# Performance work log

Measured on AMD Instinct MI355X. Metric: run time of the kernel, lower is better.

The kernel has to match this reference:

```python
import jax, jax.numpy as jnp
import numpy as np

B, D, H = 32768, 256, 256
LEAKY = 0.2  # tf.nn.leaky_relu default alpha


def setup_inputs() -> dict:
    key = jax.random.key(0)
    ks = jax.random.split(key, 12)
    s = 0.05  # weight scale (original inits comm net to zeros; random keeps grads nonzero)
    return {
        "x": jax.random.normal(ks[0], (B, D), jnp.float32),
        "visible_states_indices": jax.random.randint(ks[1], (B, 1), 0, B, jnp.int32),
        "real_step": jnp.ones((1,), jnp.bool_),
        "h": jax.random.normal(ks[2], (B, H), jnp.float32),
        "c": jax.random.normal(ks[3], (B, H), jnp.float32),
        "W1": s * jax.random.normal(ks[4], (2 * H, 512), jnp.float32),
        "b1": jnp.zeros((512,), jnp.float32),
        "W2": s * jax.random.normal(ks[5], (512, 512), jnp.float32),
        "b2": jnp.zeros((512,), jnp.float32),
        "W3": s * jax.random.normal(ks[6], (512, H), jnp.float32),
        "b3": jnp.zeros((H,), jnp.float32),
        "Wk": s * jax.random.normal(ks[7], (D, 4 * H), jnp.float32),
        "Wr": s * jax.random.normal(ks[8], (H, 4 * H), jnp.float32),
        "bl": jnp.zeros((4 * H,), jnp.float32),
    }


def reference(x, visible_states_indices, real_step, h, c,
              W1, b1, W2, b2, W3, b3, Wk, Wr, bl):
    vid = jnp.squeeze(visible_states_indices, axis=1)          # [B]
    rs = jnp.reshape(real_step, ())                            # scalar bool

    # gather neighbor comm states with a pad row for idx == -1
    padded = jnp.pad(h, ((1, 0), (0, 0)))                      # [B+1, H]
    gathered = jnp.take(padded, vid + 1, axis=0)               # [B, H]

    cs = jnp.concatenate([h, gathered], axis=-1)               # [B, 2H]
    for W, b in ((W1, b1), (W2, b2), (W3, b3)):
        cs = jax.nn.leaky_relu(cs @ W + b, negative_slope=LEAKY)

    # conditional scatter-combine back into the h state
    final_h = jnp.where((vid >= 0)[:, None], h + cs, h)        # [B, H]

    # wrapped LSTM cell (keras LSTMCell gate ordering i, f, g, o)
    z = x @ Wk + final_h @ Wr + bl                             # [B, 4H]
    i, f, g, o = jnp.split(z, 4, axis=-1)
    c_new = jax.nn.sigmoid(f) * c + jax.nn.sigmoid(i) * jnp.tanh(g)
    h_new = jax.nn.sigmoid(o) * jnp.tanh(c_new)
    outputs = h_new

    # only commit new states on real steps
    h_out = jnp.where(rs, h_new, final_h)
    c_out = jnp.where(rs, c_new, c)
    return outputs, h_out, c_out
```

## Files before the change

### kernel.cpp

```cpp
#include <hip/hip_runtime.h>
#include <stdint.h>

#define LEAKY 0.2f
#define NB 32768
#define HD 256

typedef __attribute__((ext_vector_type(8))) short short8;
typedef __attribute__((ext_vector_type(8))) unsigned short ushort8;
typedef __attribute__((ext_vector_type(4))) float f4;

static __device__ __forceinline__ float bf2f(unsigned short u) {
  union { unsigned int i; float f; } v; v.i = ((unsigned int)u) << 16; return v.f;
}
static __device__ __forceinline__ unsigned short f2bf(float f) {
  union { float f; unsigned int i; } v; v.f = f;
  return (unsigned short)((v.i + 0x7fffu + ((v.i >> 16) & 1u)) >> 16);
}
static __device__ __forceinline__ ushort8 pack8(f4 a, f4 b) {
  ushort8 o;
  o[0] = f2bf(a[0]); o[1] = f2bf(a[1]); o[2] = f2bf(a[2]); o[3] = f2bf(a[3]);
  o[4] = f2bf(b[0]); o[5] = f2bf(b[1]); o[6] = f2bf(b[2]); o[7] = f2bf(b[3]);
  return o;
}
static __device__ __forceinline__ float sigm(float x) { return 1.f / (1.f + __expf(-x)); }
static __device__ __forceinline__ float tanha(float x) {
  float e = __expf(2.f * x);
  return 1.f - 2.f / (e + 1.f);
}

__device__ __forceinline__ void gload16(const void* g, void* s) {
  __builtin_amdgcn_global_load_lds(
      (const __attribute__((address_space(1))) unsigned int*)g,
      (__attribute__((address_space(3))) unsigned int*)s, 16, 0, 0);
}

__global__ void wprep(const float* __restrict__ W1, const float* __restrict__ W2,
                      const float* __restrict__ W3, const float* __restrict__ Wk,
                      const float* __restrict__ Wr,
                      unsigned short* __restrict__ W1t, unsigned short* __restrict__ W2t,
                      unsigned short* __restrict__ W3t, unsigned short* __restrict__ Wkrt) {
  __shared__ float tile[64][65];
  const int id = blockIdx.x, t = threadIdx.x;
  const int tr = t >> 6, tc = t & 63;

  const float* src;
  unsigned short* dst;
  int kbase, nbase, srcld, perm = 0;
  if (id < 64) {
    src = W1; dst = W1t; srcld = 512;
    kbase = (id >> 3) * 64; nbase = (id & 7) * 64;
  } else if (id < 128) {
    src = W2; dst = W2t; srcld = 512;
    kbase = ((id - 64) >> 3) * 64; nbase = ((id - 64) & 7) * 64;
  } else if (id < 160) {
    src = W3; dst = W3t; srcld = 256;
    kbase = ((id - 128) >> 2) * 64; nbase = ((id - 128) & 3) * 64;
  } else {
    src = nullptr; dst = Wkrt; srcld = 1024; perm = 1;
    kbase = ((id - 160) >> 4) * 64; nbase = ((id - 160) & 15) * 64;
  }

#pragma unroll
  for (int p = 0; p < 16; ++p) {
    int r = p * 4 + tr;
    int k = kbase + r, n = nbase + tc;
    float v;
    if (perm) {
      v = (k < 256) ? Wk[k * 1024 + n] : Wr[(k - 256) * 1024 + n];
    } else {
      v = src[k * srcld + n];
    }
    tile[r][tc] = v;
  }
  __syncthreads();
#pragma unroll
  for (int p = 0; p < 16; ++p) {
    int c = p * 4 + tr;
    int n = nbase + c;
    int orow;
    if (perm) {
      int gate = n >> 8, hcol = n & 255;
      orow = (hcol >> 5) * 128 + ((hcol >> 4) & 1) * 64 + gate * 16 + (hcol & 15);
    } else {
      orow = n;
    }
    dst[orow * 512 + kbase + tc] = f2bf(tile[tc][c]);
  }
}

__global__ void build_rows(const float* __restrict__ x, const float* __restrict__ h,
                           const int* __restrict__ vid,
                           unsigned short* __restrict__ catb,
                           unsigned short* __restrict__ csb) {
  int idx = blockIdx.x * 256 + threadIdx.x;
  int m = idx >> 5;
  int j = (idx & 31) << 3;
  f4 a0 = *(const f4*)(x + (size_t)m * 256 + j);
  f4 a1 = *(const f4*)(x + (size_t)m * 256 + j + 4);
  *(ushort8*)(catb + (size_t)m * 512 + j) = pack8(a0, a1);
  f4 h0 = *(const f4*)(h + (size_t)m * 256 + j);
  f4 h1 = *(const f4*)(h + (size_t)m * 256 + j + 4);
  *(ushort8*)(csb + (size_t)m * 512 + j) = pack8(h0, h1);
  int id = vid[m];
  f4 g0 = {0.f, 0.f, 0.f, 0.f}, g1 = {0.f, 0.f, 0.f, 0.f};
  if (id >= 0) {
    g0 = *(const f4*)(h + (size_t)id * 256 + j);
    g1 = *(const f4*)(h + (size_t)id * 256 + j + 4);
  }
  *(ushort8*)(csb + (size_t)m * 512 + 256 + j) = pack8(g0, g1);
}

template <int MODE, int NTN>
__global__ __launch_bounds__(256, 4) void gemm_bf16(
    const unsigned short* __restrict__ A,
    const unsigned short* __restrict__ Bt,
    const float* __restrict__ bias,
    int K,
    unsigned short* __restrict__ outb, int ldo, int col_off,
    float* __restrict__ outf,
    const float* __restrict__ hst,
    const int* __restrict__ vid,
    const float* __restrict__ cin,
    const unsigned char* __restrict__ rsp) {
  __shared__ unsigned short sA[128 * 64];
  __shared__ unsigned short sB[128 * 64];

  const int t = threadIdx.x;
  const int p = blockIdx.x;
  const int xcd = p & 7, local = p >> 3;
  const int tm = xcd + ((local / NTN) << 3);
  const int tn = local % NTN;
  const int wid = t >> 6, lane = t & 63;
  const int wr = wid >> 1, wc = wid & 1;
  const int lrow = lane & 15, lkhi = lane >> 4;

  const unsigned short* Asrc = A + (size_t)tm * 128 * K;
  const unsigned short* Bsrc = Bt + (size_t)tn * 128 * K;
  const int rsub = t >> 3, slot = t & 7;

  f4 acc[4][4];
#pragma unroll
  for (int i = 0; i < 4; ++i)
#pragma unroll
    for (int j = 0; j < 4; ++j) acc[i][j] = {0.f, 0.f, 0.f, 0.f};

  for (int k0 = 0; k0 < K; k0 += 64) {
#pragma unroll
    for (int iss = 0; iss < 4; ++iss) {
      int r = iss * 32 + rsub;
      int gs = slot ^ (r & 7);
      gload16(Asrc + (size_t)r * K + k0 + gs * 8, (char*)sA + r * 128 + slot * 16);
      gload16(Bsrc + (size_t)r * K + k0 + gs * 8, (char*)sB + r * 128 + slot * 16);
    }
    __syncthreads();
#pragma unroll
    for (int kk = 0; kk < 2; ++kk) {
      short8 af[4], bfr[4];
#pragma unroll
      for (int mi = 0; mi < 4; ++mi) {
        int row = wr * 64 + mi * 16 + lrow;
        int s = (kk * 4 + lkhi) ^ (row & 7);
        af[mi] = *(const short8*)&sA[row * 64 + s * 8];
      }
#pragma unroll
      for (int ni = 0; ni < 4; ++ni) {
        int rn = wc * 64 + ni * 16 + lrow;
        int s = (kk * 4 + lkhi) ^ (rn & 7);
        bfr[ni] = *(const short8*)&sB[rn * 64 + s * 8];
      }
#pragma unroll
      for (int mi = 0; mi < 4; ++mi)
#pragma unroll
        for (int ni = 0; ni < 4; ++ni)
          acc[mi][ni] = __builtin_amdgcn_mfma_f32_16x16x32_bf16(af[mi], bfr[ni],
                                                                acc[mi][ni], 0, 0, 0);
    }
    __syncthreads();
  }

  const int m_base = tm * 128 + wr * 64;
  const int n_base = tn * 128 + wc * 64;
  if (MODE == 1) {
#pragma unroll
    for (int mi = 0; mi < 4; ++mi) {
#pragma unroll
      for (int r = 0; r < 4; ++r) {
        int row = m_base + mi * 16 + lkhi * 4 + r;
        int id = vid[row];
#pragma unroll
        for (int ni = 0; ni < 4; ++ni) {
          int col = n_base + ni * 16 + lrow;
          float v = acc[mi][ni][r] + bias[col];
          v = v > 0.f ? v : LEAKY * v;
          float hv = hst[(size_t)row * HD + col];
          float fh = (id >= 0) ? hv + v : hv;
          outf[(size_t)row * HD + col] = fh;
          outb[(size_t)row * ldo + col_off + col] = f2bf(fh);
        }
      }
    }
  } else if (MODE == 3) {
    const bool real = rsp[0] != 0;
    const int hcol = tn * 32 + wc * 16 + lrow;
    const float bi = bias[hcol];
    const float bff = bias[256 + hcol];
    const float bg = bias[512 + hcol];
    const float bo = bias[768 + hcol];
    float* outs = outf;
    float* houtp = outf + (size_t)NB * HD;
    float* coutp = outf + (size_t)2 * NB * HD;
#pragma unroll
    for (int mi = 0; mi < 4; ++mi) {
#pragma unroll
      for (int r = 0; r < 4; ++r) {
        int row = m_base + mi * 16 + lkhi * 4 + r;
        size_t base = (size_t)row * HD + hcol;
        float cold = cin[base];
        float i_ = sigm(acc[mi][0][r] + bi);
        float f_ = sigm(acc[mi][1][r] + bff);
        float g_ = tanha(acc[mi][2][r] + bg);
        float o_ = sigm(acc[mi][3][r] + bo);
        float cv = f_ * cold + i_ * g_;
        float hv = o_ * tanha(cv);
        outs[base] = hv;
        if (real) {
          houtp[base] = hv;
          coutp[base] = cv;
        } else {
          coutp[base] = cold;
        }
      }
    }
  } else {
#pragma unroll
    for (int ni = 0; ni < 4; ++ni) {
      int col = n_base + ni * 16 + lrow;
      float bia = bias[col];
#pragma unroll
      for (int mi = 0; mi < 4; ++mi) {
#pragma unroll
        for (int r = 0; r < 4; ++r) {
          int row = m_base + mi * 16 + lkhi * 4 + r;
          float v = acc[mi][ni][r] + bia;
          v = v > 0.f ? v : LEAKY * v;
          outb[(size_t)row * ldo + col_off + col] = f2bf(v);
        }
      }
    }
  }
}

extern "C" void kernel_launch(void* const* d_in, const int* in_sizes, int n_in,
                              void* d_out, int out_size, void* d_ws, size_t ws_size,
                              hipStream_t stream) {
  const float* x = (const float*)d_in[0];
  const int* vid = (const int*)d_in[1];
  const unsigned char* rs = (const unsigned char*)d_in[2];
  const float* h = (const float*)d_in[3];
  const float* c = (const float*)d_in[4];
  const float* W1 = (const float*)d_in[5];
  const float* b1 = (const float*)d_in[6];
  const float* W2 = (const float*)d_in[7];
  const float* b2 = (const float*)d_in[8];
  const float* W3 = (const float*)d_in[9];
  const float* b3 = (const float*)d_in[10];
  const float* Wk = (const float*)d_in[11];
  const float* Wr = (const float*)d_in[12];
  const float* bl = (const float*)d_in[13];
  float* dout = (float*)d_out;

  char* ws = (char*)d_ws;
  unsigned short* W1t = (unsigned short*)(ws);
  unsigned short* W2t = (unsigned short*)(ws + 524288);
  unsigned short* W3t = (unsigned short*)(ws + 1048576);
  unsigned short* Wkrt = (unsigned short*)(ws + 1310720);
  unsigned short* bufA = (unsigned short*)(ws + 2359296);
  unsigned short* bufB = (unsigned short*)(ws + 2359296 + 33554432);
  unsigned short* catb = (unsigned short*)(ws + 2359296 + 67108864);

  float* fhout = dout + (size_t)NB * HD;

  wprep<<<288, 256, 0, stream>>>(W1, W2, W3, Wk, Wr, W1t, W2t, W3t, Wkrt);
  build_rows<<<NB * 32 / 256, 256, 0, stream>>>(x, h, vid, catb, bufA);

  gemm_bf16<0, 4><<<(NB / 128) * 4, 256, 0, stream>>>(
      bufA, W1t, b1, 512, bufB, 512, 0, nullptr, nullptr, nullptr, nullptr, nullptr);
  gemm_bf16<0, 4><<<(NB / 128) * 4, 256, 0, stream>>>(
      bufB, W2t, b2, 512, bufA, 512, 0, nullptr, nullptr, nullptr, nullptr, nullptr);
  gemm_bf16<1, 2><<<(NB / 128) * 2, 256, 0, stream>>>(
      bufA, W3t, b3, 512, catb, 512, 256, fhout, h, vid, nullptr, nullptr);
  gemm_bf16<3, 8><<<(NB / 128) * 8, 256, 0, stream>>>(
      catb, Wkrt, bl, 512, nullptr, 0, 0, dout, nullptr, nullptr, c, rs);
}
```

Baseline: 345.2 us.

## Use 256x256 tiles with double-buffered async LDS pipeline in GEMMs

Replaces the 128x128, 4-wave GEMM with a 256x256-tile, 8-wave kernel whose K is fixed at 512. LDS is double-buffered: the next K-tile is prefetched while the current one is computed, using explicit vmcnt waits and barriers instead of a full sync before each load. Larger tiles raise arithmetic intensity per load. The cost is a 128 KB LDS footprint, heavier register use from 8x4 accumulators per wave, and fewer blocks per GEMM, which may hurt occupancy and tail balance.

```diff
diff --git a/kernel.cpp b/kernel.cpp
--- a/kernel.cpp
+++ b/kernel.cpp
@@ -111,19 +111,18 @@
 }
 
 template <int MODE, int NTN>
-__global__ __launch_bounds__(256, 4) void gemm_bf16(
+__global__ __launch_bounds__(512, 2) void gemm256(
     const unsigned short* __restrict__ A,
     const unsigned short* __restrict__ Bt,
     const float* __restrict__ bias,
-    int K,
     unsigned short* __restrict__ outb, int ldo, int col_off,
     float* __restrict__ outf,
     const float* __restrict__ hst,
     const int* __restrict__ vid,
     const float* __restrict__ cin,
     const unsigned char* __restrict__ rsp) {
-  __shared__ unsigned short sA[128 * 64];
-  __shared__ unsigned short sB[128 * 64];
+  __shared__ unsigned short sA[2][256 * 64];
+  __shared__ unsigned short sB[2][256 * 64];
 
   const int t = threadIdx.x;
   const int p = blockIdx.x;
@@ -131,58 +130,75 @@
   const int tm = xcd + ((local / NTN) << 3);
   const int tn = local % NTN;
   const int wid = t >> 6, lane = t & 63;
-  const int wr = wid >> 1, wc = wid & 1;
+  const int wr = wid >> 2, wcn = wid & 3;
   const int lrow = lane & 15, lkhi = lane >> 4;
-
-  const unsigned short* Asrc = A + (size_t)tm * 128 * K;
-  const unsigned short* Bsrc = Bt + (size_t)tn * 128 * K;
-  const int rsub = t >> 3, slot = t & 7;
-
-  f4 acc[4][4];
-#pragma unroll
-  for (int i = 0; i < 4; ++i)
+  const int rsub8 = t >> 3, slot8 = t & 7;
+
+  const unsigned short* Asrc = A + (size_t)tm * 256 * 512;
+  const unsigned short* Bsrc = Bt + (size_t)tn * 256 * 512;
+
+#define STAGE(kt, s)                                                              \
+  {                                                                               \
+    _Pragma("unroll") for (int i_ = 0; i_ < 4; ++i_) {                            \
+      int r_ = i_ * 64 + rsub8;                                                   \
+      int gs_ = slot8 ^ (r_ & 7);                                                 \
+      gload16(Asrc + (size_t)r_ * 512 + (kt) * 64 + gs_ * 8,                      \
+              (char*)&sA[s][0] + r_ * 128 + slot8 * 16);                          \
+      gload16(Bsrc + (size_t)r_ * 512 + (kt) * 64 + gs_ * 8,                      \
+              (char*)&sB[s][0] + r_ * 128 + slot8 * 16);                          \
+    }                                                                             \
+  }
+
+  f4 acc[8][4];
+#pragma unroll
+  for (int i = 0; i < 8; ++i)
 #pragma unroll
     for (int j = 0; j < 4; ++j) acc[i][j] = {0.f, 0.f, 0.f, 0.f};
 
-  for (int k0 = 0; k0 < K; k0 += 64) {
-#pragma unroll
-    for (int iss = 0; iss < 4; ++iss) {
-      int r = iss * 32 + rsub;
-      int gs = slot ^ (r & 7);
-      gload16(Asrc + (size_t)r * K + k0 + gs * 8, (char*)sA + r * 128 + slot * 16);
-      gload16(Bsrc + (size_t)r * K + k0 + gs * 8, (char*)sB + r * 128 + slot * 16);
-    }
-    __syncthreads();
+  STAGE(0, 0)
+  STAGE(1, 1)
+
+#pragma unroll
+  for (int kt = 0; kt < 8; ++kt) {
+    const int cur = kt & 1;
+    if (kt < 7) {
+      asm volatile("s_waitcnt vmcnt(8)" ::: "memory");
+    } else {
+      asm volatile("s_waitcnt vmcnt(0)" ::: "memory");
+    }
+    __builtin_amdgcn_s_barrier();
+    __builtin_amdgcn_sched_barrier(0);
 #pragma unroll
     for (int kk = 0; kk < 2; ++kk) {
-      short8 af[4], bfr[4];
-#pragma unroll
-      for (int mi = 0; mi < 4; ++mi) {
-        int row = wr * 64 + mi * 16 + lrow;
+      short8 bfr[4];
+#pragma unroll
+      for (int ni = 0; ni < 4; ++ni) {
+        int rn = wcn * 64 + ni * 16 + lrow;
+        int s = (kk * 4 + lkhi) ^ (rn & 7);
+        bfr[ni] = *(const short8*)&sB[cur][rn * 64 + s * 8];
+      }
+#pragma unroll
+      for (int mi = 0; mi < 8; ++mi) {
+        int row = wr * 128 + mi * 16 + lrow;
         int s = (kk * 4 + lkhi) ^ (row & 7);
-        af[mi] = *(const short8*)&sA[row * 64 + s * 8];
-      }
-#pragma unroll
-      for (int ni = 0; ni < 4; ++ni) {
-        int rn = wc * 64 + ni * 16 + lrow;
-        int s = (kk * 4 + lkhi) ^ (rn & 7);
-        bfr[ni] = *(const short8*)&sB[rn * 64 + s * 8];
-      }
-#pragma unroll
-      for (int mi = 0; mi < 4; ++mi)
+        short8 a = *(const short8*)&sA[cur][row * 64 + s * 8];
 #pragma unroll
         for (int ni = 0; ni < 4; ++ni)
-          acc[mi][ni] = __builtin_amdgcn_mfma_f32_16x16x32_bf16(af[mi], bfr[ni],
+          acc[mi][ni] = __builtin_amdgcn_mfma_f32_16x16x32_bf16(a, bfr[ni],
                                                                 acc[mi][ni], 0, 0, 0);
-    }
-    __syncthreads();
-  }
-
-  const int m_base = tm * 128 + wr * 64;
-  const int n_base = tn * 128 + wc * 64;
+      }
+    }
+    __builtin_amdgcn_s_barrier();
+    __builtin_amdgcn_sched_barrier(0);
+    if (kt + 2 < 8) STAGE(kt + 2, cur)
+  }
+#undef STAGE
+
+  const int m_base = tm * 256 + wr * 128;
+  const int n_base = tn * 256 + wcn * 64;
   if (MODE == 1) {
 #pragma unroll
-    for (int mi = 0; mi < 4; ++mi) {
+    for (int mi = 0; mi < 8; ++mi) {
 #pragma unroll
       for (int r = 0; r < 4; ++r) {
         int row = m_base + mi * 16 + lkhi * 4 + r;
@@ -201,7 +217,7 @@
     }
   } else if (MODE == 3) {
     const bool real = rsp[0] != 0;
-    const int hcol = tn * 32 + wc * 16 + lrow;
+    const int hcol = (tn * 2 + (wcn >> 1)) * 32 + (wcn & 1) * 16 + lrow;
     const float bi = bias[hcol];
     const float bff = bias[256 + hcol];
     const float bg = bias[512 + hcol];
@@ -210,7 +226,7 @@
     float* houtp = outf + (size_t)NB * HD;
     float* coutp = outf + (size_t)2 * NB * HD;
 #pragma unroll
-    for (int mi = 0; mi < 4; ++mi) {
+    for (int mi = 0; mi < 8; ++mi) {
 #pragma unroll
       for (int r = 0; r < 4; ++r) {
         int row = m_base + mi * 16 + lkhi * 4 + r;
@@ -237,7 +253,7 @@
       int col = n_base + ni * 16 + lrow;
       float bia = bias[col];
 #pragma unroll
-      for (int mi = 0; mi < 4; ++mi) {
+      for (int mi = 0; mi < 8; ++mi) {
 #pragma unroll
         for (int r = 0; r < 4; ++r) {
           int row = m_base + mi * 16 + lkhi * 4 + r;
@@ -283,12 +299,12 @@
   wprep<<<288, 256, 0, stream>>>(W1, W2, W3, Wk, Wr, W1t, W2t, W3t, Wkrt);
   build_rows<<<NB * 32 / 256, 256, 0, stream>>>(x, h, vid, catb, bufA);
 
-  gemm_bf16<0, 4><<<(NB / 128) * 4, 256, 0, stream>>>(
-      bufA, W1t, b1, 512, bufB, 512, 0, nullptr, nullptr, nullptr, nullptr, nullptr);
-  gemm_bf16<0, 4><<<(NB / 128) * 4, 256, 0, stream>>>(
-      bufB, W2t, b2, 512, bufA, 512, 0, nullptr, nullptr, nullptr, nullptr, nullptr);
-  gemm_bf16<1, 2><<<(NB / 128) * 2, 256, 0, stream>>>(
-      bufA, W3t, b3, 512, catb, 512, 256, fhout, h, vid, nullptr, nullptr);
-  gemm_bf16<3, 8><<<(NB / 128) * 8, 256, 0, stream>>>(
-      catb, Wkrt, bl, 512, nullptr, 0, 0, dout, nullptr, nullptr, c, rs);
-}
+  gemm256<0, 2><<<(NB / 256) * 2, 512, 0, stream>>>(
+      bufA, W1t, b1, bufB, 512, 0, nullptr, nullptr, nullptr, nullptr, nullptr);
+  gemm256<0, 2><<<(NB / 256) * 2, 512, 0, stream>>>(
+      bufB, W2t, b2, bufA, 512, 0, nullptr, nullptr, nullptr, nullptr, nullptr);
+  gemm256<1, 1><<<(NB / 256) * 1, 512, 0, stream>>>(
+      bufA, W3t, b3, catb, 512, 256, fhout, h, vid, nullptr, nullptr);
+  gemm256<3, 4><<<(NB / 256) * 4, 512, 0, stream>>>(
+      catb, Wkrt, bl, nullptr, 0, 0, dout, nullptr, nullptr, c, rs);
+}
```

Result: slower. 376.5 us (+9.0%).

## Pipeline GEMM K-loop with 4-stage async LDS buffering at BK=32

Applied to the files above, without the earlier changes.

Replaces the single-buffered BK=64 GEMM loop with a 4-deep ring of BK=32 LDS stages, prefetching three tiles ahead. Manual vmcnt waits and one barrier per step replace the two syncthreads per iteration. The goal is to hide global-to-LDS load latency behind MFMA work. K is now hardcoded to 512, launch bounds drop to 2 blocks per CU, and the swizzle pattern changes to fit the narrower tiles.

```diff
diff --git a/kernel.cpp b/kernel.cpp
--- a/kernel.cpp
+++ b/kernel.cpp
@@ -111,19 +111,18 @@
 }
 
 template <int MODE, int NTN>
-__global__ __launch_bounds__(256, 4) void gemm_bf16(
+__global__ __launch_bounds__(256, 2) void gemm_bk32(
     const unsigned short* __restrict__ A,
     const unsigned short* __restrict__ Bt,
     const float* __restrict__ bias,
-    int K,
     unsigned short* __restrict__ outb, int ldo, int col_off,
     float* __restrict__ outf,
     const float* __restrict__ hst,
     const int* __restrict__ vid,
     const float* __restrict__ cin,
     const unsigned char* __restrict__ rsp) {
-  __shared__ unsigned short sA[128 * 64];
-  __shared__ unsigned short sB[128 * 64];
+  __shared__ unsigned short sA[4][128 * 32];
+  __shared__ unsigned short sB[4][128 * 32];
 
   const int t = threadIdx.x;
   const int p = blockIdx.x;
@@ -134,9 +133,25 @@
   const int wr = wid >> 1, wc = wid & 1;
   const int lrow = lane & 15, lkhi = lane >> 4;
 
-  const unsigned short* Asrc = A + (size_t)tm * 128 * K;
-  const unsigned short* Bsrc = Bt + (size_t)tn * 128 * K;
-  const int rsub = t >> 3, slot = t & 7;
+  const unsigned short* Asrc = A + (size_t)tm * 128 * 512;
+  const unsigned short* Bsrc = Bt + (size_t)tn * 128 * 512;
+
+  const int r0 = t >> 2, sl0 = t & 3;
+  const int r1 = (256 + t) >> 2, sl1 = sl0;
+  const int gs0 = sl0 ^ ((r0 & 3) ^ ((r0 >> 2) & 3));
+  const int gs1 = sl1 ^ ((r1 & 3) ^ ((r1 >> 2) & 3));
+
+#define STAGE(kt, s)                                                          \
+  {                                                                           \
+    gload16(Asrc + (size_t)r0 * 512 + (kt) * 32 + gs0 * 8,                    \
+            (char*)&sA[s][0] + t * 16);                                       \
+    gload16(Bsrc + (size_t)r0 * 512 + (kt) * 32 + gs0 * 8,                    \
+            (char*)&sB[s][0] + t * 16);                                       \
+    gload16(Asrc + (size_t)r1 * 512 + (kt) * 32 + gs1 * 8,                    \
+            (char*)&sA[s][0] + 4096 + t * 16);                                \
+    gload16(Bsrc + (size_t)r1 * 512 + (kt) * 32 + gs1 * 8,                    \
+            (char*)&sB[s][0] + 4096 + t * 16);                                \
+  }
 
   f4 acc[4][4];
 #pragma unroll
@@ -144,39 +159,44 @@
 #pragma unroll
     for (int j = 0; j < 4; ++j) acc[i][j] = {0.f, 0.f, 0.f, 0.f};
 
-  for (int k0 = 0; k0 < K; k0 += 64) {
-#pragma unroll
-    for (int iss = 0; iss < 4; ++iss) {
-      int r = iss * 32 + rsub;
-      int gs = slot ^ (r & 7);
-      gload16(Asrc + (size_t)r * K + k0 + gs * 8, (char*)sA + r * 128 + slot * 16);
-      gload16(Bsrc + (size_t)r * K + k0 + gs * 8, (char*)sB + r * 128 + slot * 16);
-    }
-    __syncthreads();
-#pragma unroll
-    for (int kk = 0; kk < 2; ++kk) {
-      short8 af[4], bfr[4];
-#pragma unroll
-      for (int mi = 0; mi < 4; ++mi) {
-        int row = wr * 64 + mi * 16 + lrow;
-        int s = (kk * 4 + lkhi) ^ (row & 7);
-        af[mi] = *(const short8*)&sA[row * 64 + s * 8];
-      }
-#pragma unroll
-      for (int ni = 0; ni < 4; ++ni) {
-        int rn = wc * 64 + ni * 16 + lrow;
-        int s = (kk * 4 + lkhi) ^ (rn & 7);
-        bfr[ni] = *(const short8*)&sB[rn * 64 + s * 8];
-      }
-#pragma unroll
-      for (int mi = 0; mi < 4; ++mi)
-#pragma unroll
-        for (int ni = 0; ni < 4; ++ni)
-          acc[mi][ni] = __builtin_amdgcn_mfma_f32_16x16x32_bf16(af[mi], bfr[ni],
-                                                                acc[mi][ni], 0, 0, 0);
-    }
-    __syncthreads();
-  }
+  STAGE(0, 0) STAGE(1, 1) STAGE(2, 2)
+
+#pragma unroll
+  for (int T = 0; T < 16; ++T) {
+    const int cur = T & 3;
+    if (T <= 13) {
+      asm volatile("s_waitcnt vmcnt(8)" ::: "memory");
+    } else if (T == 14) {
+      asm volatile("s_waitcnt vmcnt(4)" ::: "memory");
+    } else {
+      asm volatile("s_waitcnt vmcnt(0)" ::: "memory");
+    }
+    __builtin_amdgcn_s_barrier();
+    __builtin_amdgcn_sched_barrier(0);
+    if (T + 3 < 16) STAGE(T + 3, (T + 3) & 3)
+    __builtin_amdgcn_sched_barrier(0);
+
+    short8 af[4], bfr[4];
+#pragma unroll
+    for (int mi = 0; mi < 4; ++mi) {
+      int row = wr * 64 + mi * 16 + lrow;
+      int f = (row & 3) ^ ((row >> 2) & 3);
+      af[mi] = *(const short8*)&sA[cur][row * 32 + ((lkhi ^ f) << 3)];
+    }
+#pragma unroll
+    for (int ni = 0; ni < 4; ++ni) {
+      int rn = wc * 64 + ni * 16 + lrow;
+      int f = (rn & 3) ^ ((rn >> 2) & 3);
+      bfr[ni] = *(const short8*)&sB[cur][rn * 32 + ((lkhi ^ f) << 3)];
+    }
+#pragma unroll
+    for (int mi = 0; mi < 4; ++mi)
+#pragma unroll
+      for (int ni = 0; ni < 4; ++ni)
+        acc[mi][ni] = __builtin_amdgcn_mfma_f32_16x16x32_bf16(af[mi], bfr[ni],
+                                                              acc[mi][ni], 0, 0, 0);
+  }
+#undef STAGE
 
   const int m_base = tm * 128 + wr * 64;
   const int n_base = tn * 128 + wc * 64;
@@ -283,12 +303,12 @@
   wprep<<<288, 256, 0, stream>>>(W1, W2, W3, Wk, Wr, W1t, W2t, W3t, Wkrt);
   build_rows<<<NB * 32 / 256, 256, 0, stream>>>(x, h, vid, catb, bufA);
 
-  gemm_bf16<0, 4><<<(NB / 128) * 4, 256, 0, stream>>>(
-      bufA, W1t, b1, 512, bufB, 512, 0, nullptr, nullptr, nullptr, nullptr, nullptr);
-  gemm_bf16<0, 4><<<(NB / 128) * 4, 256, 0, stream>>>(
-      bufB, W2t, b2, 512, bufA, 512, 0, nullptr, nullptr, nullptr, nullptr, nullptr);
-  gemm_bf16<1, 2><<<(NB / 128) * 2, 256, 0, stream>>>(
-      bufA, W3t, b3, 512, catb, 512, 256, fhout, h, vid, nullptr, nullptr);
-  gemm_bf16<3, 8><<<(NB / 128) * 8, 256, 0, stream>>>(
-      catb, Wkrt, bl, 512, nullptr, 0, 0, dout, nullptr, nullptr, c, rs);
-}
+  gemm_bk32<0, 4><<<(NB / 128) * 4, 256, 0, stream>>>(
+      bufA, W1t, b1, bufB, 512, 0, nullptr, nullptr, nullptr, nullptr, nullptr);
+  gemm_bk32<0, 4><<<(NB / 128) * 4, 256, 0, stream>>>(
+      bufB, W2t, b2, bufA, 512, 0, nullptr, nullptr, nullptr, nullptr, nullptr);
+  gemm_bk32<1, 2><<<(NB / 128) * 2, 256, 0, stream>>>(
+      bufA, W3t, b3, catb, 512, 256, fhout, h, vid, nullptr, nullptr);
+  gemm_bk32<3, 8><<<(NB / 128) * 8, 256, 0, stream>>>(
+      catb, Wkrt, bl, nullptr, 0, 0, dout, nullptr, nullptr, c, rs);
+}
```

Measured after the change: 363.2 us. +5.2%, slower.
